# Kernel tuning notes

Measured on AMD Instinct MI355X. Metric: run time of the kernel, lower is better.

The kernel has to match this reference:

```python
import jax, jax.numpy as jnp
import numpy as np

N_R = 256          # number of relations
N_HOP_MAX = 3      # max hops
N_E = 200_000      # number of entities
N_T = 1_000_000    # number of KB triples
B = 32             # batch size
D_Q = 768          # BERT question embedding dim
D_IN = D_Q + (N_HOP_MAX - 1) * N_R  # input width of dense_inf / dense_att


def setup_inputs() -> dict:
    key = jax.random.key(0)
    ks = jax.random.split(key, 7)
    x = (jax.random.uniform(ks[0], (B, N_E)) < 0.001).astype(jnp.float32)
    h_q = jax.random.normal(ks[1], (B, D_Q), jnp.float32)
    W_inf = jax.random.normal(ks[2], (N_R, D_IN), jnp.float32) * 0.02
    W_att = jax.random.normal(ks[3], (1, D_IN), jnp.float32) * 0.02
    subj_idx = jax.random.randint(ks[4], (N_T,), 0, N_E, jnp.int32)
    rel_idx = jax.random.randint(ks[5], (N_T,), 0, N_R, jnp.int32)
    obj_idx = jax.random.randint(ks[6], (N_T,), 0, N_E, jnp.int32)
    return {"x": x, "h_q": h_q, "W_inf": W_inf, "W_att": W_att,
            "subj_idx": subj_idx, "rel_idx": rel_idx, "obj_idx": obj_idx,
            "n_hop": N_HOP_MAX}


def _one_step(x, r, subj_idx, rel_idx, obj_idx):
    # Equivalent to ((x @ M_subj.T) * (r @ M_rel.T)) @ M_obj with 0/1
    # indicator matrices: gather - elementwise multiply - scatter-add.
    x_t = jnp.take(x, subj_idx, axis=1)   # (B, N_T)
    r_t = jnp.take(r, rel_idx, axis=1)    # (B, N_T)
    prod = x_t * r_t                       # (B, N_T)
    # scatter-add over triples into object entities: (N_T, B) -> (N_E, B)
    return jax.ops.segment_sum(prod.T, obj_idx, num_segments=x.shape[1]).T


def reference(x, h_q, W_inf, W_att, subj_idx, rel_idx, obj_idx, n_hop):
    rs, cs, xs = [], [], []
    for i in range(n_hop):
        if i:
            # most-recent relation first, then older ones (rs[::-1])
            concat = jnp.concatenate([h_q] + rs[::-1], axis=1)
        else:
            concat = h_q
        pad = jnp.zeros((h_q.shape[0], (N_HOP_MAX - 1 - i) * N_R), h_q.dtype)
        concat = jnp.concatenate([concat, pad], axis=1)  # (B, D_IN)
        r = concat @ W_inf.T   # (B, N_R)
        c = concat @ W_att.T   # (B, 1)
        x = _one_step(x, r, subj_idx, rel_idx, obj_idx)  # (B, N_E)
        rs.append(r)
        cs.append(c)
        xs.append(x)
    a = jax.nn.softmax(jnp.concatenate(cs, axis=1), axis=-1)  # (B, n_hop)
    y = jnp.einsum('bh,bhe->be', a, jnp.stack(xs, axis=1))     # (B, N_E)
    return y
```

## Files before the change

### kernel.cpp

```cpp
#include <hip/hip_runtime.h>

#define N_R   256
#define N_E   200000
#define N_T   1000000
#define D_Q   768
#define D_IN  1280
#define NHB   3907

template <bool BN, bool WM>
__device__ __forceinline__ void hop_one(
        const float* __restrict__ xIn, const unsigned* __restrict__ maskIn,
        const float* __restrict__ rT,
        const int* __restrict__ subj, const int* __restrict__ rel,
        const int* __restrict__ obj,
        float* __restrict__ xOut, unsigned* __restrict__ maskOut, int tid) {
    if (tid >= N_T) return;
    int s = subj[tid];
    int r = rel[tid];
    int o = obj[tid];
    unsigned mm = maskIn[s];
    if (!mm) return;
    if (WM) atomicOr(&maskOut[o], mm);
    const float* rrow = rT + r * 32;
    while (mm) {
        int bb = __ffs(mm) - 1;
        mm &= mm - 1;
        float v = BN ? xIn[(size_t)bb * N_E + s] : xIn[(size_t)s * 32 + bb];
        unsafeAtomicAdd(&xOut[(size_t)o * 32 + bb], v * rrow[bb]);
    }
}

__global__ void kA(const float* __restrict__ x, const float* __restrict__ h_q,
                   const float* __restrict__ W_inf,
                   unsigned* __restrict__ mask0, unsigned* __restrict__ mask1,
                   unsigned* __restrict__ mask2,
                   float4* __restrict__ bufC4, float* __restrict__ rT0) {
    __shared__ float hs[32 * 257];
    __shared__ float red[256];
    int t = threadIdx.x;
    if (blockIdx.x < 782) {
        int tid = blockIdx.x * 256 + t;
        float4 z = {0.f, 0.f, 0.f, 0.f};
        for (int i = tid; i < 1600000; i += 782 * 256) bufC4[i] = z;
        if (tid < N_E) {
            unsigned m = 0;
#pragma unroll 8
            for (int b = 0; b < 32; ++b)
                m |= (x[(size_t)b * N_E + tid] != 0.f ? 1u : 0u) << b;
            mask0[tid] = m;
            mask1[tid] = 0u;
            mask2[tid] = 0u;
        }
    } else {
        int rel = blockIdx.x - 782;
        int b = t & 31, kp = t >> 5;
        float acc = 0.f;
        for (int c = 0; c < 3; ++c) {
            __syncthreads();
#pragma unroll
            for (int i = 0; i < 32; ++i)
                hs[i * 257 + t] = h_q[i * D_Q + c * 256 + t];
            __syncthreads();
            const float* w = &W_inf[rel * D_IN + c * 256 + kp * 32];
#pragma unroll
            for (int i = 0; i < 32; ++i)
                acc += w[i] * hs[b * 257 + kp * 32 + i];
        }
        red[t] = acc;
        __syncthreads();
        if (t < 32) {
            float s = 0.f;
            for (int q = 0; q < 8; ++q) s += red[q * 32 + t];
            rT0[rel * 32 + t] = s;
        }
    }
}

__global__ void kB(const float* __restrict__ W_inf, const float* __restrict__ rT0,
                   float* __restrict__ rT1,
                   const float* __restrict__ x, const unsigned* __restrict__ mask0,
                   const int* __restrict__ subj, const int* __restrict__ rel,
                   const int* __restrict__ obj,
                   float* __restrict__ bufA, unsigned* __restrict__ mask1) {
    __shared__ float red[256];
    int t = threadIdx.x;
    if (blockIdx.x < 256) {
        int relb = blockIdx.x;
        int b = t & 31, jp = t >> 5;
        const float* w2 = &W_inf[relb * D_IN + D_Q];
        float acc = 0.f;
#pragma unroll 8
        for (int jj = 0; jj < 32; ++jj) {
            int j = jp * 32 + jj;
            acc += w2[j] * rT0[j * 32 + b];
        }
        red[t] = acc;
        __syncthreads();
        if (t < 32) {
            float s = rT0[relb * 32 + t];
            for (int q = 0; q < 8; ++q) s += red[q * 32 + t];
            rT1[relb * 32 + t] = s;
        }
    } else {
        hop_one<true, true>(x, mask0, rT0, subj, rel, obj, bufA, mask1,
                            (blockIdx.x - 256) * 256 + t);
    }
}

__global__ void kC(const float* __restrict__ W_inf, const float* __restrict__ W_att,
                   const float* __restrict__ h_q,
                   const float* __restrict__ rT0, const float* __restrict__ rT1,
                   float* __restrict__ rT2, float* __restrict__ a_w,
                   const float* __restrict__ bufA, const unsigned* __restrict__ mask1,
                   const int* __restrict__ subj, const int* __restrict__ rel,
                   const int* __restrict__ obj,
                   float* __restrict__ bufB, unsigned* __restrict__ mask2) {
    __shared__ float red[256];
    __shared__ float p0[256], p1[256], p2[256], p3[256];
    int t = threadIdx.x;
    if (blockIdx.x < 256) {
        int relb = blockIdx.x;
        int b = t & 31, jp = t >> 5;
        const float* w2 = &W_inf[relb * D_IN + D_Q];
        const float* w3 = w2 + N_R;
        float acc = 0.f;
#pragma unroll 8
        for (int jj = 0; jj < 32; ++jj) {
            int j = jp * 32 + jj;
            acc += w2[j] * rT1[j * 32 + b] + w3[j] * rT0[j * 32 + b];
        }
        red[t] = acc;
        __syncthreads();
        if (t < 32) {
            float s = rT0[relb * 32 + t];
            for (int q = 0; q < 8; ++q) s += red[q * 32 + t];
            rT2[relb * 32 + t] = s;
        }
    } else if (blockIdx.x == 256) {
        int b = t & 31, p = t >> 5;
        float c0 = 0.f;
        for (int k = p * 96; k < p * 96 + 96; ++k) c0 += W_att[k] * h_q[b * D_Q + k];
        float s1 = 0.f, s2 = 0.f, s3 = 0.f;
        for (int j = p * 32; j < p * 32 + 32; ++j) {
            float w2 = W_att[D_Q + j], w3 = W_att[D_Q + N_R + j];
            float r0v = rT0[j * 32 + b], r1v = rT1[j * 32 + b];
            s1 += w2 * r0v; s2 += w2 * r1v; s3 += w3 * r0v;
        }
        p0[t] = c0; p1[t] = s1; p2[t] = s2; p3[t] = s3;
        __syncthreads();
        if (t < 32) {
            float C0 = 0.f, S1 = 0.f, S2 = 0.f, S3 = 0.f;
            for (int q = 0; q < 8; ++q) {
                C0 += p0[q * 32 + t]; S1 += p1[q * 32 + t];
                S2 += p2[q * 32 + t]; S3 += p3[q * 32 + t];
            }
            float c1 = C0 + S1, c2 = C0 + S2 + S3;
            float m  = fmaxf(C0, fmaxf(c1, c2));
            float e0 = __expf(C0 - m), e1 = __expf(c1 - m), e2 = __expf(c2 - m);
            float inv = 1.f / (e0 + e1 + e2);
            a_w[t] = e0 * inv; a_w[32 + t] = e1 * inv; a_w[64 + t] = e2 * inv;
        }
    } else {
        hop_one<false, true>(bufA, mask1, rT1, subj, rel, obj, bufB, mask2,
                             (blockIdx.x - 257) * 256 + t);
    }
}

__global__ void kD(const float* __restrict__ bufB, const unsigned* __restrict__ mask2,
                   const float* __restrict__ rT2,
                   const int* __restrict__ subj, const int* __restrict__ rel,
                   const int* __restrict__ obj, float* __restrict__ bufC) {
    hop_one<false, false>(bufB, mask2, rT2, subj, rel, obj, bufC, nullptr,
                          blockIdx.x * 256 + threadIdx.x);
}

__global__ void kE(const float* __restrict__ bufA, const float* __restrict__ bufB,
                   const float* __restrict__ bufC,
                   const unsigned* __restrict__ mask1,
                   const unsigned* __restrict__ mask2,
                   const float* __restrict__ a_w, float* __restrict__ out) {
    __shared__ float tile[256 * 33];
    __shared__ unsigned m1s[256], m2s[256];
    __shared__ float aw[96];
    int t = threadIdx.x;
    int e0 = blockIdx.x * 256;
    if (t < 96) aw[t] = a_w[t];
    {
        int e = e0 + t;
        m1s[t] = (e < N_E) ? mask1[e] : 0u;
        m2s[t] = (e < N_E) ? mask2[e] : 0u;
    }
    __syncthreads();
    size_t base = (size_t)e0 * 32;
#pragma unroll
    for (int i = 0; i < 32; ++i) {
        int idx = i * 256 + t;
        int el = idx >> 5, b = idx & 31;
        float v = 0.f;
        if (e0 + el < N_E) {
            v = aw[64 + b] * bufC[base + idx];
            unsigned mm1 = m1s[el], mm2 = m2s[el];
            if ((mm1 >> b) & 1) v += aw[b]      * bufA[base + idx];
            if ((mm2 >> b) & 1) v += aw[32 + b] * bufB[base + idx];
        }
        tile[el * 33 + b] = v;
    }
    __syncthreads();
    int e = e0 + t;
    if (e < N_E) {
#pragma unroll
        for (int i = 0; i < 32; ++i)
            out[(size_t)i * N_E + e] = tile[t * 33 + i];
    }
}

extern "C" void kernel_launch(void* const* d_in, const int* in_sizes, int n_in,
                              void* d_out, int out_size, void* d_ws, size_t ws_size,
                              hipStream_t stream) {
    const float* x     = (const float*)d_in[0];
    const float* h_q   = (const float*)d_in[1];
    const float* W_inf = (const float*)d_in[2];
    const float* W_att = (const float*)d_in[3];
    const int*   subj  = (const int*)d_in[4];
    const int*   rel   = (const int*)d_in[5];
    const int*   obj   = (const int*)d_in[6];
    float* out = (float*)d_out;

    const size_t NEB = (size_t)N_E * 32;
    float*    bufA  = (float*)d_ws;
    float*    bufB  = bufA + NEB;
    float*    bufC  = bufB + NEB;
    float*    rT0   = bufC + NEB;
    float*    rT1   = rT0 + N_R * 32;
    float*    rT2   = rT1 + N_R * 32;
    float*    a_w   = rT2 + N_R * 32;
    unsigned* mask0 = (unsigned*)(a_w + 96);
    unsigned* mask1 = mask0 + N_E;
    unsigned* mask2 = mask1 + N_E;

    kA<<<782 + 256, 256, 0, stream>>>(x, h_q, W_inf, mask0, mask1, mask2,
                                      (float4*)bufC, rT0);
    kB<<<256 + NHB, 256, 0, stream>>>(W_inf, rT0, rT1, x, mask0,
                                      subj, rel, obj, bufA, mask1);
    kC<<<257 + NHB, 256, 0, stream>>>(W_inf, W_att, h_q, rT0, rT1, rT2, a_w,
                                      bufA, mask1, subj, rel, obj, bufB, mask2);
    kD<<<NHB, 256, 0, stream>>>(bufB, mask2, rT2, subj, rel, obj, bufC);
    kE<<<782, 256, 0, stream>>>(bufA, bufB, bufC, mask1, mask2, a_w, out);
}
```

Before: 204.0 us.

## Add entity bitsets for early-out and fuse last hop with output combine

Adds a compact per-entity activity bitset (one bit per entity) built with a wave ballot and updated by atomicOr, so each triple checks a small cached word before loading rel/obj and the per-entity mask. The third hop now scatters directly into the output in batch-major layout, already scaled by its attention weight. The separate final combine kernel and the bufC buffer are replaced by a pass that atomically adds only the active hop-1 and hop-2 contributions into the output. This removes one full-size buffer zero and read plus a dense transpose pass, at the cost of more scattered atomics into strided output rows and extra bitset atomics.

```diff
diff --git a/kernel.cpp b/kernel.cpp
--- a/kernel.cpp
+++ b/kernel.cpp
@@ -6,21 +6,25 @@
 #define D_Q   768
 #define D_IN  1280
 #define NHB   3907
-
-template <bool BN, bool WM>
+#define NBW   6256
+
+template <bool BN>
 __device__ __forceinline__ void hop_one(
         const float* __restrict__ xIn, const unsigned* __restrict__ maskIn,
-        const float* __restrict__ rT,
+        const unsigned* __restrict__ bitIn, const float* __restrict__ rT,
         const int* __restrict__ subj, const int* __restrict__ rel,
         const int* __restrict__ obj,
-        float* __restrict__ xOut, unsigned* __restrict__ maskOut, int tid) {
+        float* __restrict__ xOut, unsigned* __restrict__ maskOut,
+        unsigned* __restrict__ bitOut, int tid) {
     if (tid >= N_T) return;
     int s = subj[tid];
+    unsigned gw = bitIn[s >> 5];
+    if (!((gw >> (s & 31)) & 1)) return;
     int r = rel[tid];
     int o = obj[tid];
     unsigned mm = maskIn[s];
-    if (!mm) return;
-    if (WM) atomicOr(&maskOut[o], mm);
+    atomicOr(&maskOut[o], mm);
+    atomicOr(&bitOut[o >> 5], 1u << (o & 31));
     const float* rrow = rT + r * 32;
     while (mm) {
         int bb = __ffs(mm) - 1;
@@ -34,19 +38,28 @@
                    const float* __restrict__ W_inf,
                    unsigned* __restrict__ mask0, unsigned* __restrict__ mask1,
                    unsigned* __restrict__ mask2,
-                   float4* __restrict__ bufC4, float* __restrict__ rT0) {
+                   unsigned* __restrict__ bit0, unsigned* __restrict__ bit1,
+                   unsigned* __restrict__ bit2,
+                   float4* __restrict__ outv, float* __restrict__ rT0) {
     __shared__ float hs[32 * 257];
     __shared__ float red[256];
     int t = threadIdx.x;
     if (blockIdx.x < 782) {
         int tid = blockIdx.x * 256 + t;
         float4 z = {0.f, 0.f, 0.f, 0.f};
-        for (int i = tid; i < 1600000; i += 782 * 256) bufC4[i] = z;
+        for (int i = tid; i < 1600000; i += 782 * 256) outv[i] = z;
+        if (tid < NBW) { bit1[tid] = 0u; bit2[tid] = 0u; }
+        unsigned m = 0;
         if (tid < N_E) {
-            unsigned m = 0;
 #pragma unroll 8
             for (int b = 0; b < 32; ++b)
                 m |= (x[(size_t)b * N_E + tid] != 0.f ? 1u : 0u) << b;
+        }
+        unsigned long long bal = __ballot(m != 0u);
+        int lane = t & 63;
+        if (lane == 0)  bit0[tid >> 5] = (unsigned)bal;
+        if (lane == 32) bit0[tid >> 5] = (unsigned)(bal >> 32);
+        if (tid < N_E) {
             mask0[tid] = m;
             mask1[tid] = 0u;
             mask2[tid] = 0u;
@@ -79,9 +92,11 @@
 __global__ void kB(const float* __restrict__ W_inf, const float* __restrict__ rT0,
                    float* __restrict__ rT1,
                    const float* __restrict__ x, const unsigned* __restrict__ mask0,
+                   const unsigned* __restrict__ bit0,
                    const int* __restrict__ subj, const int* __restrict__ rel,
                    const int* __restrict__ obj,
-                   float* __restrict__ bufA, unsigned* __restrict__ mask1) {
+                   float* __restrict__ bufA, unsigned* __restrict__ mask1,
+                   unsigned* __restrict__ bit1) {
     __shared__ float red[256];
     int t = threadIdx.x;
     if (blockIdx.x < 256) {
@@ -102,8 +117,8 @@
             rT1[relb * 32 + t] = s;
         }
     } else {
-        hop_one<true, true>(x, mask0, rT0, subj, rel, obj, bufA, mask1,
-                            (blockIdx.x - 256) * 256 + t);
+        hop_one<true>(x, mask0, bit0, rT0, subj, rel, obj, bufA, mask1, bit1,
+                      (blockIdx.x - 256) * 256 + t);
     }
 }
 
@@ -112,9 +127,11 @@
                    const float* __restrict__ rT0, const float* __restrict__ rT1,
                    float* __restrict__ rT2, float* __restrict__ a_w,
                    const float* __restrict__ bufA, const unsigned* __restrict__ mask1,
+                   const unsigned* __restrict__ bit1,
                    const int* __restrict__ subj, const int* __restrict__ rel,
                    const int* __restrict__ obj,
-                   float* __restrict__ bufB, unsigned* __restrict__ mask2) {
+                   float* __restrict__ bufB, unsigned* __restrict__ mask2,
+                   unsigned* __restrict__ bit2) {
     __shared__ float red[256];
     __shared__ float p0[256], p1[256], p2[256], p3[256];
     int t = threadIdx.x;
@@ -161,56 +178,55 @@
             a_w[t] = e0 * inv; a_w[32 + t] = e1 * inv; a_w[64 + t] = e2 * inv;
         }
     } else {
-        hop_one<false, true>(bufA, mask1, rT1, subj, rel, obj, bufB, mask2,
-                             (blockIdx.x - 257) * 256 + t);
-    }
-}
-
-__global__ void kD(const float* __restrict__ bufB, const unsigned* __restrict__ mask2,
-                   const float* __restrict__ rT2,
-                   const int* __restrict__ subj, const int* __restrict__ rel,
-                   const int* __restrict__ obj, float* __restrict__ bufC) {
-    hop_one<false, false>(bufB, mask2, rT2, subj, rel, obj, bufC, nullptr,
-                          blockIdx.x * 256 + threadIdx.x);
-}
-
-__global__ void kE(const float* __restrict__ bufA, const float* __restrict__ bufB,
-                   const float* __restrict__ bufC,
-                   const unsigned* __restrict__ mask1,
-                   const unsigned* __restrict__ mask2,
-                   const float* __restrict__ a_w, float* __restrict__ out) {
-    __shared__ float tile[256 * 33];
-    __shared__ unsigned m1s[256], m2s[256];
-    __shared__ float aw[96];
-    int t = threadIdx.x;
-    int e0 = blockIdx.x * 256;
-    if (t < 96) aw[t] = a_w[t];
-    {
-        int e = e0 + t;
-        m1s[t] = (e < N_E) ? mask1[e] : 0u;
-        m2s[t] = (e < N_E) ? mask2[e] : 0u;
-    }
+        hop_one<false>(bufA, mask1, bit1, rT1, subj, rel, obj, bufB, mask2, bit2,
+                       (blockIdx.x - 257) * 256 + t);
+    }
+}
+
+__global__ void kDE(const float* __restrict__ bufA, const float* __restrict__ bufB,
+                    const unsigned* __restrict__ mask1,
+                    const unsigned* __restrict__ mask2,
+                    const unsigned* __restrict__ bit2,
+                    const float* __restrict__ rT2, const float* __restrict__ a_w,
+                    const int* __restrict__ subj, const int* __restrict__ rel,
+                    const int* __restrict__ obj, float* __restrict__ out) {
+    __shared__ float a0s[32], a1s[32], a2s[32];
+    int t = threadIdx.x;
+    if (t < 32) { a0s[t] = a_w[t]; a1s[t] = a_w[32 + t]; a2s[t] = a_w[64 + t]; }
     __syncthreads();
-    size_t base = (size_t)e0 * 32;
-#pragma unroll
-    for (int i = 0; i < 32; ++i) {
-        int idx = i * 256 + t;
-        int el = idx >> 5, b = idx & 31;
-        float v = 0.f;
-        if (e0 + el < N_E) {
-            v = aw[64 + b] * bufC[base + idx];
-            unsigned mm1 = m1s[el], mm2 = m2s[el];
-            if ((mm1 >> b) & 1) v += aw[b]      * bufA[base + idx];
-            if ((mm2 >> b) & 1) v += aw[32 + b] * bufB[base + idx];
-        }
-        tile[el * 33 + b] = v;
-    }
-    __syncthreads();
-    int e = e0 + t;
-    if (e < N_E) {
-#pragma unroll
-        for (int i = 0; i < 32; ++i)
-            out[(size_t)i * N_E + e] = tile[t * 33 + i];
+    if (blockIdx.x < NHB) {
+        int tid = blockIdx.x * 256 + t;
+        if (tid >= N_T) return;
+        int s = subj[tid];
+        int r = rel[tid];
+        int o = obj[tid];
+        unsigned gw = bit2[s >> 5];
+        if (!((gw >> (s & 31)) & 1)) return;
+        unsigned mm = mask2[s];
+        const float* rrow = rT2 + r * 32;
+        const float* xrow = bufB + (size_t)s * 32;
+        while (mm) {
+            int bb = __ffs(mm) - 1;
+            mm &= mm - 1;
+            unsafeAtomicAdd(&out[(size_t)bb * N_E + o],
+                            a2s[bb] * xrow[bb] * rrow[bb]);
+        }
+    } else {
+        int e = (blockIdx.x - NHB) * 256 + t;
+        if (e >= N_E) return;
+        unsigned m1v = mask1[e], m2v = mask2[e];
+        unsigned mu = m1v | m2v;
+        if (!mu) return;
+        const float* r1 = bufA + (size_t)e * 32;
+        const float* r2 = bufB + (size_t)e * 32;
+        while (mu) {
+            int bb = __ffs(mu) - 1;
+            mu &= mu - 1;
+            float c = 0.f;
+            if ((m1v >> bb) & 1) c += a0s[bb] * r1[bb];
+            if ((m2v >> bb) & 1) c += a1s[bb] * r2[bb];
+            unsafeAtomicAdd(&out[(size_t)bb * N_E + e], c);
+        }
     }
 }
 
@@ -229,21 +245,24 @@
     const size_t NEB = (size_t)N_E * 32;
     float*    bufA  = (float*)d_ws;
     float*    bufB  = bufA + NEB;
-    float*    bufC  = bufB + NEB;
-    float*    rT0   = bufC + NEB;
+    float*    rT0   = bufB + NEB;
     float*    rT1   = rT0 + N_R * 32;
     float*    rT2   = rT1 + N_R * 32;
     float*    a_w   = rT2 + N_R * 32;
     unsigned* mask0 = (unsigned*)(a_w + 96);
     unsigned* mask1 = mask0 + N_E;
     unsigned* mask2 = mask1 + N_E;
+    unsigned* bit0  = mask2 + N_E;
+    unsigned* bit1  = bit0 + NBW;
+    unsigned* bit2  = bit1 + NBW;
 
     kA<<<782 + 256, 256, 0, stream>>>(x, h_q, W_inf, mask0, mask1, mask2,
-                                      (float4*)bufC, rT0);
-    kB<<<256 + NHB, 256, 0, stream>>>(W_inf, rT0, rT1, x, mask0,
-                                      subj, rel, obj, bufA, mask1);
+                                      bit0, bit1, bit2, (float4*)out, rT0);
+    kB<<<256 + NHB, 256, 0, stream>>>(W_inf, rT0, rT1, x, mask0, bit0,
+                                      subj, rel, obj, bufA, mask1, bit1);
     kC<<<257 + NHB, 256, 0, stream>>>(W_inf, W_att, h_q, rT0, rT1, rT2, a_w,
-                                      bufA, mask1, subj, rel, obj, bufB, mask2);
-    kD<<<NHB, 256, 0, stream>>>(bufB, mask2, rT2, subj, rel, obj, bufC);
-    kE<<<782, 256, 0, stream>>>(bufA, bufB, bufC, mask1, mask2, a_w, out);
-}
+                                      bufA, mask1, bit1, subj, rel, obj,
+                                      bufB, mask2, bit2);
+    kDE<<<NHB + 782, 256, 0, stream>>>(bufA, bufB, mask1, mask2, bit2, rT2, a_w,
+                                       subj, rel, obj, out);
+}
```

Measured after the change: 194.3 us. 4.7% less time.
